# Performance work log

Hardware: AMD Instinct MI355X
Metric: run time of the kernel (lower is better)

Reference implementation:

```python
import jax, jax.numpy as jnp
import numpy as np

FEAT_DIM, M, K, D = 1024, 32, 256, 32
B = 8192
ALPHA = 1.0
BN_EPS = 1e-5
NORM_EPS = 1e-12  # F.normalize eps


def _l2_normalize(v, axis=-1):
    # matches torch F.normalize: v / max(||v||, eps)
    n = jnp.sqrt(jnp.sum(v * v, axis=axis, keepdims=True))
    return v / jnp.maximum(n, NORM_EPS)


def setup_inputs() -> dict:
    key = jax.random.key(0)
    kx, kc = jax.random.split(key)
    x = jax.random.normal(kx, (B, FEAT_DIM), dtype=jnp.float32)
    # xavier-uniform init over (M,K,D) then per-codeword L2 normalization (as in __init__)
    limit = float(np.sqrt(6.0 / (K + D)))
    C_k = jax.random.uniform(kc, (M, K, D), dtype=jnp.float32, minval=-limit, maxval=limit)
    C_k = _l2_normalize(C_k, axis=-1)
    return {"x": x, "C_k": C_k}


def reference(x, C_k):
    Bn = x.shape[0]
    x_ = x.reshape(Bn, M, D)                       # (B, M, D)
    x_norm_ = _l2_normalize(x_, axis=-1)           # per-subspace normalize
    x_normalized = x_norm_.reshape(Bn, FEAT_DIM)

    # per-subspace similarity: (B, M, K)
    sims = jnp.einsum('bmd,mkd->bmk', x_norm_, C_k)

    # BatchNorm1d(M, affine=False) in training mode: normalize per channel m over (B, K)
    mean = jnp.mean(sims, axis=(0, 2), keepdims=True)
    var = jnp.mean(jnp.square(sims - mean), axis=(0, 2), keepdims=True)  # biased var
    sims = (sims - mean) / jnp.sqrt(var + BN_EPS)

    # hard assignment + codeword gather (C_v == C_k in VQ mode)
    hard_codes = jnp.argmax(sims, axis=-1)                     # (B, M) int
    x_hat_hard_ = C_k[jnp.arange(M)[None, :], hard_codes]      # (B, M, D)
    x_hat_hard = x_hat_hard_.reshape(Bn, FEAT_DIM)

    # soft assignment (mask_topK is None)
    soft_codes = jax.nn.softmax(sims * ALPHA, axis=-1)         # (B, M, K)

    # straight-through: value = x_hat_hard, grad flows through x_normalized
    x_hat = x_normalized - jax.lax.stop_gradient(x_normalized - x_hat_hard)

    # pq_detach_opt == 'features'
    reg_loss = jnp.sum(jnp.square(jax.lax.stop_gradient(x_normalized) - x_hat_hard), axis=-1)  # (B,)

    return (x_hat, hard_codes, soft_codes, x_normalized, reg_loss)
```

## Files before the change

### kernel.cpp

```cpp
#include <hip/hip_runtime.h>
#include <cmath>

#define FEAT_DIM 1024
#define MM 32
#define KK 256
#define DD 32
#define BB 8192

constexpr float BN_EPS = 1e-5f;

typedef float f32x4 __attribute__((ext_vector_type(4)));

__device__ __forceinline__ float wave_fsum(float v) {
    #pragma unroll
    for (int s = 32; s >= 1; s >>= 1) v += __shfl_xor(v, s);
    return v;
}

template <int CTRL, int RM = 0xf>
__device__ __forceinline__ float dppf(float v) {
    int r = __builtin_amdgcn_update_dpp(__builtin_bit_cast(int, v),
                                        __builtin_bit_cast(int, v),
                                        CTRL, RM, 0xf, false);
    return __builtin_bit_cast(float, r);
}
__device__ __forceinline__ float wave_dpp_max(float v) {
    v = fmaxf(v, dppf<0xB1>(v));
    v = fmaxf(v, dppf<0x4E>(v));
    v = fmaxf(v, dppf<0x141>(v));
    v = fmaxf(v, dppf<0x140>(v));
    v = fmaxf(v, dppf<0x142, 0xa>(v));
    v = fmaxf(v, dppf<0x143, 0xc>(v));
    return __builtin_bit_cast(float, __builtin_amdgcn_readlane(__builtin_bit_cast(int, v), 63));
}
__device__ __forceinline__ float wave_dpp_sum(float v) {
    v += dppf<0xB1>(v);
    v += dppf<0x4E>(v);
    v += dppf<0x141>(v);
    v += dppf<0x140>(v);
    v += dppf<0x142, 0xa>(v);
    v += dppf<0x143, 0xc>(v);
    return __builtin_bit_cast(float, __builtin_amdgcn_readlane(__builtin_bit_cast(int, v), 63));
}

__global__ void k_norm(const float* __restrict__ x, float* __restrict__ xn,
                       double* __restrict__ stats) {
    if (blockIdx.x == 0 && threadIdx.x < 2 * MM) stats[threadIdx.x] = 0.0;
    const int t = blockIdx.x * blockDim.x + threadIdx.x;
    float4 v = ((const float4*)x)[t];
    float ss = v.x*v.x + v.y*v.y + v.z*v.z + v.w*v.w;
    #pragma unroll
    for (int s = 1; s < 8; s <<= 1) ss += __shfl_xor(ss, s);
    const float r = 1.0f / fmaxf(sqrtf(ss), 1e-12f);
    float4 o = {v.x*r, v.y*r, v.z*r, v.w*r};
    ((float4*)xn)[t] = o;
}

__global__ void k_gram(const float* __restrict__ Ck, float* __restrict__ G,
                       float* __restrict__ S) {
    __shared__ float CT[DD][KK + 4];
    const int m = blockIdx.x, part = blockIdx.y;
    const int t = threadIdx.x, wid = t >> 6, lane = t & 63;
    const float4* cp = (const float4*)(Ck + ((size_t)m * KK + t) * DD);
    #pragma unroll
    for (int i = 0; i < 8; ++i) {
        float4 v = cp[i];
        CT[4*i+0][t] = v.x; CT[4*i+1][t] = v.y;
        CT[4*i+2][t] = v.z; CT[4*i+3][t] = v.w;
    }
    __syncthreads();
    #pragma unroll 1
    for (int ei = 0; ei < 32; ++ei) {
        const int e = part * 128 + wid * 32 + ei;
        const int i = e >> 5, j = e & 31;
        float acc = 0.f;
        #pragma unroll
        for (int c4 = 0; c4 < 4; ++c4)
            acc = fmaf(CT[i][lane + 64*c4], CT[j][lane + 64*c4], acc);
        acc = wave_fsum(acc);
        if (lane == 0) G[((size_t)m * DD + i) * DD + j] = acc;
    }
    if (part == 0 && wid == 0) {
        #pragma unroll 1
        for (int d = 0; d < DD; ++d) {
            float a = 0.f;
            #pragma unroll
            for (int c4 = 0; c4 < 4; ++c4) a += CT[d][lane + 64*c4];
            a = wave_fsum(a);
            if (lane == 0) S[m * DD + d] = a;
        }
    }
}

__global__ void k_stats2(const float* __restrict__ xn, const float* __restrict__ G,
                         const float* __restrict__ S, double* __restrict__ stats) {
    const int m = blockIdx.x;
    const int b = blockIdx.y * 256 + threadIdx.x;
    float xv[DD];
    {
        const float4* xp = (const float4*)(xn + (size_t)b * FEAT_DIM + m * DD);
        #pragma unroll
        for (int i = 0; i < 8; ++i) {
            float4 v = xp[i];
            xv[4*i+0]=v.x; xv[4*i+1]=v.y; xv[4*i+2]=v.z; xv[4*i+3]=v.w;
        }
    }
    const float4* Gp = (const float4*)(G + (size_t)m * DD * DD);
    const float*  Sp = S + m * DD;
    float q = 0.f, s = 0.f;
    #pragma unroll 4
    for (int i = 0; i < DD; ++i) {
        float y = 0.f;
        #pragma unroll
        for (int jv = 0; jv < 8; ++jv) {
            float4 g = Gp[i * 8 + jv];
            y = fmaf(g.x, xv[4*jv+0], y); y = fmaf(g.y, xv[4*jv+1], y);
            y = fmaf(g.z, xv[4*jv+2], y); y = fmaf(g.w, xv[4*jv+3], y);
        }
        q = fmaf(y, xv[i], q);
    }
    #pragma unroll
    for (int i = 0; i < DD; ++i) s = fmaf(Sp[i], xv[i], s);
    q = wave_fsum(q); s = wave_fsum(s);
    __shared__ float lq[4], ls[4];
    const int wid = threadIdx.x >> 6, lane = threadIdx.x & 63;
    if (lane == 0) { lq[wid] = q; ls[wid] = s; }
    __syncthreads();
    if (threadIdx.x == 0) {
        atomicAdd(&stats[2*m],   (double)((ls[0]+ls[1])+(ls[2]+ls[3])));
        atomicAdd(&stats[2*m+1], (double)((lq[0]+lq[1])+(lq[2]+lq[3])));
    }
}

template <int BT>
__global__ __launch_bounds__(256)
__attribute__((amdgpu_waves_per_eu(2, 2)))
void k_main(const float* __restrict__ xn, const float* __restrict__ Ck,
            const double* __restrict__ stats,
            float* __restrict__ xhat, float* __restrict__ hard,
            float* __restrict__ soft, float* __restrict__ part) {
    const int m = blockIdx.x;
    const int wid = threadIdx.x >> 6, lane = threadIdx.x & 63;

    const double Ninv = 1.0 / ((double)BB * (double)KK);
    const double mu  = stats[2*m] * Ninv;
    const double var = stats[2*m+1] * Ninv - mu * mu;
    const float rstd = (float)(1.0 / sqrt(var + (double)BN_EPS));
    const float c1 = rstd * 1.4426950408889634f;

    float c[4][DD];
    #pragma unroll
    for (int j = 0; j < 4; ++j) {
        const float4* cp = (const float4*)(Ck + ((size_t)m * KK + 4*lane + j) * DD);
        #pragma unroll
        for (int i = 0; i < 8; ++i) {
            float4 v = cp[i];
            c[j][4*i+0]=v.x; c[j][4*i+1]=v.y; c[j][4*i+2]=v.z; c[j][4*i+3]=v.w;
        }
    }

    const int b_base = blockIdx.y * (4 * BT) + wid;

    auto loadslice = [&](float4 (&q)[8], int b) {
        const int bu = __builtin_amdgcn_readfirstlane(b);
        const float4* xp = (const float4*)(xn + (size_t)bu * FEAT_DIM + m * DD);
        #pragma unroll
        for (int i = 0; i < 8; ++i) q[i] = xp[i];
    };

    auto process = [&](const float4 (&q)[8], int b) {
        float d0=0.f, d1=0.f, d2=0.f, d3=0.f;
        #pragma unroll
        for (int i = 0; i < 8; ++i) {
            const float4 q4 = q[i];
            d0 = fmaf(q4.x, c[0][4*i+0], d0); d0 = fmaf(q4.y, c[0][4*i+1], d0);
            d0 = fmaf(q4.z, c[0][4*i+2], d0); d0 = fmaf(q4.w, c[0][4*i+3], d0);
            d1 = fmaf(q4.x, c[1][4*i+0], d1); d1 = fmaf(q4.y, c[1][4*i+1], d1);
            d1 = fmaf(q4.z, c[1][4*i+2], d1); d1 = fmaf(q4.w, c[1][4*i+3], d1);
            d2 = fmaf(q4.x, c[2][4*i+0], d2); d2 = fmaf(q4.y, c[2][4*i+1], d2);
            d2 = fmaf(q4.z, c[2][4*i+2], d2); d2 = fmaf(q4.w, c[2][4*i+3], d2);
            d3 = fmaf(q4.x, c[3][4*i+0], d3); d3 = fmaf(q4.y, c[3][4*i+1], d3);
            d3 = fmaf(q4.z, c[3][4*i+2], d3); d3 = fmaf(q4.w, c[3][4*i+3], d3);
        }

        const float p0 = exp2f(d0 * c1);
        const float p1 = exp2f(d1 * c1);
        const float p2 = exp2f(d2 * c1);
        const float p3 = exp2f(d3 * c1);

        const float mx = wave_dpp_max(fmaxf(fmaxf(d0, d1), fmaxf(d2, d3)));
        const unsigned long long m0 = __ballot(d0 == mx);
        const unsigned long long m1 = __ballot(d1 == mx);
        const unsigned long long m2 = __ballot(d2 == mx);
        const unsigned long long m3 = __ballot(d3 == mx);
        const int k0 = m0 ? 4*__builtin_ctzll(m0)+0 : 0x7fffffff;
        const int k1 = m1 ? 4*__builtin_ctzll(m1)+1 : 0x7fffffff;
        const int k2 = m2 ? 4*__builtin_ctzll(m2)+2 : 0x7fffffff;
        const int k3 = m3 ? 4*__builtin_ctzll(m3)+3 : 0x7fffffff;
        const int bi = min(min(k0, k1), min(k2, k3));

        const float tot = wave_dpp_sum((p0 + p1) + (p2 + p3));
        const float inv = __builtin_amdgcn_rcpf(tot);

        f32x4 o = {p0*inv, p1*inv, p2*inv, p3*inv};
        __builtin_nontemporal_store(o, (f32x4*)(soft + ((size_t)b * MM + m) * KK) + lane);
        if (lane == 0) {
            hard[(size_t)b * MM + m] = (float)bi;
            part[(size_t)m * BB + b] = 2.f - 2.f * mx;
        }
        if (lane < 8) {
            f32x4 cw = ((const f32x4*)(Ck + ((size_t)m * KK + bi) * DD))[lane];
            __builtin_nontemporal_store(cw, (f32x4*)(xhat + (size_t)b * FEAT_DIM + m * DD) + lane);
        }
    };

    float4 A[8], Bv[8];
    loadslice(A, b_base);
    #pragma unroll 1
    for (int it = 0; it < BT; it += 2) {
        loadslice(Bv, b_base + 4 * (it + 1));
        process(A, b_base + 4 * it);
        if (it + 2 < BT) loadslice(A, b_base + 4 * (it + 2));
        process(Bv, b_base + 4 * (it + 1));
    }
}

__global__ void k_regsum(const float* __restrict__ part, float* __restrict__ reg) {
    const int b = blockIdx.x * 256 + threadIdx.x;
    float a = 0.f;
    #pragma unroll
    for (int mm = 0; mm < MM; ++mm) a += part[(size_t)mm * BB + b];
    reg[b] = a;
}

extern "C" void kernel_launch(void* const* d_in, const int* in_sizes, int n_in,
                              void* d_out, int out_size, void* d_ws, size_t ws_size,
                              hipStream_t stream) {
    const float* x  = (const float*)d_in[0];
    const float* Ck = (const float*)d_in[1];

    float* out   = (float*)d_out;
    float* xhat  = out;
    float* hard  = xhat  + (size_t)BB * FEAT_DIM;
    float* soft  = hard  + (size_t)BB * MM;
    float* xnorm = soft  + (size_t)BB * MM * KK;
    float* reg   = xnorm + (size_t)BB * FEAT_DIM;

    double* stats = (double*)d_ws;
    float* partb  = (float*)d_ws + 256;
    float* Gbuf = soft;
    float* Sbuf = soft + (size_t)MM * DD * DD;

    k_norm<<<(BB * FEAT_DIM / 4) / 256, 256, 0, stream>>>(x, xnorm, stats);
    k_gram<<<dim3(MM, 8), 256, 0, stream>>>(Ck, Gbuf, Sbuf);
    k_stats2<<<dim3(MM, BB / 256), 256, 0, stream>>>(xnorm, Gbuf, Sbuf, stats);
    constexpr int BT = 32;
    k_main<BT><<<dim3(MM, BB / (4 * BT)), 256, 0, stream>>>(xnorm, Ck, stats, xhat, hard, soft, partb);
    k_regsum<<<BB / 256, 256, 0, stream>>>(partb, reg);
}
```

Before: 194.2 us.

## Load wave-uniform x slices via scalar loads into SGPRs and raise occupancy

The per-batch 32-float x slice is wave-uniform, so it is now fetched with s_load_dwordx16 into scalar registers instead of per-lane vector loads, with a double-buffered prefetch and explicit lgkmcnt waits. This frees vector registers and removes redundant vector-memory traffic, which lets the wave occupancy target rise from 2 to 3 waves per EU. The prefetch clamps the row index to stay in bounds, and the explicit waitcnt plus sched_barrier may limit overlap with other LGKM traffic such as DPP/readlane usage.

```diff
diff --git a/kernel.cpp b/kernel.cpp
--- a/kernel.cpp
+++ b/kernel.cpp
@@ -9,7 +9,8 @@
 
 constexpr float BN_EPS = 1e-5f;
 
-typedef float f32x4 __attribute__((ext_vector_type(4)));
+typedef float f32x4  __attribute__((ext_vector_type(4)));
+typedef float f32x16 __attribute__((ext_vector_type(16)));
 
 __device__ __forceinline__ float wave_fsum(float v) {
     #pragma unroll
@@ -41,6 +42,16 @@
     v += dppf<0x142, 0xa>(v);
     v += dppf<0x143, 0xc>(v);
     return __builtin_bit_cast(float, __builtin_amdgcn_readlane(__builtin_bit_cast(int, v), 63));
+}
+
+__device__ __forceinline__ void sload_slice(f32x16& lo, f32x16& hi, const float* p) {
+    asm volatile("s_load_dwordx16 %0, %2, 0x0\n\t"
+                 "s_load_dwordx16 %1, %2, 0x40"
+                 : "=s"(lo), "=s"(hi) : "s"(p));
+}
+__device__ __forceinline__ void swait(f32x16& lo, f32x16& hi) {
+    asm volatile("s_waitcnt lgkmcnt(0)" : "+s"(lo), "+s"(hi));
+    __builtin_amdgcn_sched_barrier(0);
 }
 
 __global__ void k_norm(const float* __restrict__ x, float* __restrict__ xn,
@@ -134,7 +145,7 @@
 
 template <int BT>
 __global__ __launch_bounds__(256)
-__attribute__((amdgpu_waves_per_eu(2, 2)))
+__attribute__((amdgpu_waves_per_eu(3, 3)))
 void k_main(const float* __restrict__ xn, const float* __restrict__ Ck,
             const double* __restrict__ stats,
             float* __restrict__ xhat, float* __restrict__ hard,
@@ -161,26 +172,39 @@
 
     const int b_base = blockIdx.y * (4 * BT) + wid;
 
-    auto loadslice = [&](float4 (&q)[8], int b) {
+    auto slice_ptr = [&](int it) {
+        int b = b_base + 4 * it;
+        b = min(b, BB - 1);
         const int bu = __builtin_amdgcn_readfirstlane(b);
-        const float4* xp = (const float4*)(xn + (size_t)bu * FEAT_DIM + m * DD);
-        #pragma unroll
-        for (int i = 0; i < 8; ++i) q[i] = xp[i];
+        return xn + (size_t)bu * FEAT_DIM + m * DD;
     };
 
-    auto process = [&](const float4 (&q)[8], int b) {
+    auto process = [&](const f32x16& lo, const f32x16& hi, int b) {
         float d0=0.f, d1=0.f, d2=0.f, d3=0.f;
         #pragma unroll
-        for (int i = 0; i < 8; ++i) {
-            const float4 q4 = q[i];
-            d0 = fmaf(q4.x, c[0][4*i+0], d0); d0 = fmaf(q4.y, c[0][4*i+1], d0);
-            d0 = fmaf(q4.z, c[0][4*i+2], d0); d0 = fmaf(q4.w, c[0][4*i+3], d0);
-            d1 = fmaf(q4.x, c[1][4*i+0], d1); d1 = fmaf(q4.y, c[1][4*i+1], d1);
-            d1 = fmaf(q4.z, c[1][4*i+2], d1); d1 = fmaf(q4.w, c[1][4*i+3], d1);
-            d2 = fmaf(q4.x, c[2][4*i+0], d2); d2 = fmaf(q4.y, c[2][4*i+1], d2);
-            d2 = fmaf(q4.z, c[2][4*i+2], d2); d2 = fmaf(q4.w, c[2][4*i+3], d2);
-            d3 = fmaf(q4.x, c[3][4*i+0], d3); d3 = fmaf(q4.y, c[3][4*i+1], d3);
-            d3 = fmaf(q4.z, c[3][4*i+2], d3); d3 = fmaf(q4.w, c[3][4*i+3], d3);
+        for (int i = 0; i < 4; ++i) {
+            const float x0 = lo[4*i+0], x1 = lo[4*i+1], x2 = lo[4*i+2], x3 = lo[4*i+3];
+            d0 = fmaf(x0, c[0][4*i+0], d0); d0 = fmaf(x1, c[0][4*i+1], d0);
+            d0 = fmaf(x2, c[0][4*i+2], d0); d0 = fmaf(x3, c[0][4*i+3], d0);
+            d1 = fmaf(x0, c[1][4*i+0], d1); d1 = fmaf(x1, c[1][4*i+1], d1);
+            d1 = fmaf(x2, c[1][4*i+2], d1); d1 = fmaf(x3, c[1][4*i+3], d1);
+            d2 = fmaf(x0, c[2][4*i+0], d2); d2 = fmaf(x1, c[2][4*i+1], d2);
+            d2 = fmaf(x2, c[2][4*i+2], d2); d2 = fmaf(x3, c[2][4*i+3], d2);
+            d3 = fmaf(x0, c[3][4*i+0], d3); d3 = fmaf(x1, c[3][4*i+1], d3);
+            d3 = fmaf(x2, c[3][4*i+2], d3); d3 = fmaf(x3, c[3][4*i+3], d3);
+        }
+        #pragma unroll
+        for (int i = 4; i < 8; ++i) {
+            const int e = 4 * (i - 4);
+            const float x0 = hi[e+0], x1 = hi[e+1], x2 = hi[e+2], x3 = hi[e+3];
+            d0 = fmaf(x0, c[0][4*i+0], d0); d0 = fmaf(x1, c[0][4*i+1], d0);
+            d0 = fmaf(x2, c[0][4*i+2], d0); d0 = fmaf(x3, c[0][4*i+3], d0);
+            d1 = fmaf(x0, c[1][4*i+0], d1); d1 = fmaf(x1, c[1][4*i+1], d1);
+            d1 = fmaf(x2, c[1][4*i+2], d1); d1 = fmaf(x3, c[1][4*i+3], d1);
+            d2 = fmaf(x0, c[2][4*i+0], d2); d2 = fmaf(x1, c[2][4*i+1], d2);
+            d2 = fmaf(x2, c[2][4*i+2], d2); d2 = fmaf(x3, c[2][4*i+3], d2);
+            d3 = fmaf(x0, c[3][4*i+0], d3); d3 = fmaf(x1, c[3][4*i+1], d3);
+            d3 = fmaf(x2, c[3][4*i+2], d3); d3 = fmaf(x3, c[3][4*i+3], d3);
         }
 
         const float p0 = exp2f(d0 * c1);
@@ -214,14 +238,17 @@
         }
     };
 
-    float4 A[8], Bv[8];
-    loadslice(A, b_base);
+    f32x16 alo, ahi, blo, bhi;
+    sload_slice(alo, ahi, slice_ptr(0));
+    sload_slice(blo, bhi, slice_ptr(1));
     #pragma unroll 1
     for (int it = 0; it < BT; it += 2) {
-        loadslice(Bv, b_base + 4 * (it + 1));
-        process(A, b_base + 4 * it);
-        if (it + 2 < BT) loadslice(A, b_base + 4 * (it + 2));
-        process(Bv, b_base + 4 * (it + 1));
+        swait(alo, ahi);
+        process(alo, ahi, b_base + 4 * it);
+        sload_slice(alo, ahi, slice_ptr(it + 2));
+        swait(blo, bhi);
+        process(blo, bhi, b_base + 4 * (it + 1));
+        sload_slice(blo, bhi, slice_ptr(it + 3));
     }
 }
 
```

After: 179.0 us. 7.8% less time.

## Fuse normalization into stats kernel and write xhat from register codewords

Applied to the files above, without the earlier changes.

Removes the separate normalization kernel: the stats kernel now reads raw x, normalizes each 32-wide subspace per thread, writes xnorm, and scales the quadratic and linear terms by the inverse norm. This saves one full read of x and one launch. The xhat gather no longer loads the codeword from global memory; the lane that owns the argmax codeword stores it from registers. The launch attribute also changes from waves_per_eu(2,2) to launch_bounds(256,2), which may alter register allocation. Moving the stats zeroing into k_gram keeps it ordered before the atomics.

```diff
diff --git a/kernel.cpp b/kernel.cpp
--- a/kernel.cpp
+++ b/kernel.cpp
@@ -43,24 +43,12 @@
     return __builtin_bit_cast(float, __builtin_amdgcn_readlane(__builtin_bit_cast(int, v), 63));
 }
 
-__global__ void k_norm(const float* __restrict__ x, float* __restrict__ xn,
-                       double* __restrict__ stats) {
-    if (blockIdx.x == 0 && threadIdx.x < 2 * MM) stats[threadIdx.x] = 0.0;
-    const int t = blockIdx.x * blockDim.x + threadIdx.x;
-    float4 v = ((const float4*)x)[t];
-    float ss = v.x*v.x + v.y*v.y + v.z*v.z + v.w*v.w;
-    #pragma unroll
-    for (int s = 1; s < 8; s <<= 1) ss += __shfl_xor(ss, s);
-    const float r = 1.0f / fmaxf(sqrtf(ss), 1e-12f);
-    float4 o = {v.x*r, v.y*r, v.z*r, v.w*r};
-    ((float4*)xn)[t] = o;
-}
-
 __global__ void k_gram(const float* __restrict__ Ck, float* __restrict__ G,
-                       float* __restrict__ S) {
+                       float* __restrict__ S, double* __restrict__ stats) {
     __shared__ float CT[DD][KK + 4];
     const int m = blockIdx.x, part = blockIdx.y;
     const int t = threadIdx.x, wid = t >> 6, lane = t & 63;
+    if (m == 0 && part == 0 && t < 2 * MM) stats[t] = 0.0;
     const float4* cp = (const float4*)(Ck + ((size_t)m * KK + t) * DD);
     #pragma unroll
     for (int i = 0; i < 8; ++i) {
@@ -92,17 +80,30 @@
     }
 }
 
-__global__ void k_stats2(const float* __restrict__ xn, const float* __restrict__ G,
-                         const float* __restrict__ S, double* __restrict__ stats) {
+__global__ void k_ns(const float* __restrict__ x, float* __restrict__ xn,
+                     const float* __restrict__ G, const float* __restrict__ S,
+                     double* __restrict__ stats) {
     const int m = blockIdx.x;
     const int b = blockIdx.y * 256 + threadIdx.x;
     float xv[DD];
     {
-        const float4* xp = (const float4*)(xn + (size_t)b * FEAT_DIM + m * DD);
+        const float4* xp = (const float4*)(x + (size_t)b * FEAT_DIM + m * DD);
         #pragma unroll
         for (int i = 0; i < 8; ++i) {
             float4 v = xp[i];
             xv[4*i+0]=v.x; xv[4*i+1]=v.y; xv[4*i+2]=v.z; xv[4*i+3]=v.w;
+        }
+    }
+    float ss = 0.f;
+    #pragma unroll
+    for (int i = 0; i < DD; ++i) ss = fmaf(xv[i], xv[i], ss);
+    const float rn = 1.0f / fmaxf(sqrtf(ss), 1e-12f);
+    {
+        float4* op = (float4*)(xn + (size_t)b * FEAT_DIM + m * DD);
+        #pragma unroll
+        for (int i = 0; i < 8; ++i) {
+            float4 o = {xv[4*i+0]*rn, xv[4*i+1]*rn, xv[4*i+2]*rn, xv[4*i+3]*rn};
+            op[i] = o;
         }
     }
     const float4* Gp = (const float4*)(G + (size_t)m * DD * DD);
@@ -121,6 +122,8 @@
     }
     #pragma unroll
     for (int i = 0; i < DD; ++i) s = fmaf(Sp[i], xv[i], s);
+    q = q * rn * rn;
+    s = s * rn;
     q = wave_fsum(q); s = wave_fsum(s);
     __shared__ float lq[4], ls[4];
     const int wid = threadIdx.x >> 6, lane = threadIdx.x & 63;
@@ -133,8 +136,7 @@
 }
 
 template <int BT>
-__global__ __launch_bounds__(256)
-__attribute__((amdgpu_waves_per_eu(2, 2)))
+__global__ __launch_bounds__(256, 2)
 void k_main(const float* __restrict__ xn, const float* __restrict__ Ck,
             const double* __restrict__ stats,
             float* __restrict__ xhat, float* __restrict__ hard,
@@ -208,9 +210,16 @@
             hard[(size_t)b * MM + m] = (float)bi;
             part[(size_t)m * BB + b] = 2.f - 2.f * mx;
         }
-        if (lane < 8) {
-            f32x4 cw = ((const f32x4*)(Ck + ((size_t)m * KK + bi) * DD))[lane];
-            __builtin_nontemporal_store(cw, (f32x4*)(xhat + (size_t)b * FEAT_DIM + m * DD) + lane);
+        #pragma unroll
+        for (int j = 0; j < 4; ++j) {
+            if (4 * lane + j == bi) {
+                f32x4* xp = (f32x4*)(xhat + (size_t)b * FEAT_DIM + m * DD);
+                #pragma unroll
+                for (int i = 0; i < 8; ++i) {
+                    f32x4 cw = {c[j][4*i+0], c[j][4*i+1], c[j][4*i+2], c[j][4*i+3]};
+                    __builtin_nontemporal_store(cw, xp + i);
+                }
+            }
         }
     };
 
@@ -251,9 +260,8 @@
     float* Gbuf = soft;
     float* Sbuf = soft + (size_t)MM * DD * DD;
 
-    k_norm<<<(BB * FEAT_DIM / 4) / 256, 256, 0, stream>>>(x, xnorm, stats);
-    k_gram<<<dim3(MM, 8), 256, 0, stream>>>(Ck, Gbuf, Sbuf);
-    k_stats2<<<dim3(MM, BB / 256), 256, 0, stream>>>(xnorm, Gbuf, Sbuf, stats);
+    k_gram<<<dim3(MM, 8), 256, 0, stream>>>(Ck, Gbuf, Sbuf, stats);
+    k_ns<<<dim3(MM, BB / 256), 256, 0, stream>>>(x, xnorm, Gbuf, Sbuf, stats);
     constexpr int BT = 32;
     k_main<BT><<<dim3(MM, BB / (4 * BT)), 256, 0, stream>>>(xnorm, Ck, stats, xhat, hard, soft, partb);
     k_regsum<<<BB / 256, 256, 0, stream>>>(partb, reg);
```

After: 222.2 us. +14.4%, slower.
